# Performance work log

Measured on AMD Instinct MI355X. Metric: run time of the kernel, lower is better.

## Reference

```python
import jax, jax.numpy as jnp
import numpy as np

B, L, D, S = 64, 512, 768, 8
HOP, LAMB = 3, 0.5


def _layernorm(x, g, b, eps=1e-5):
    m = x.mean(-1, keepdims=True)
    v = x.var(-1, keepdims=True)
    return (x - m) / jnp.sqrt(v + eps) * g + b


def _hop_refine(cur, sentence, ln_g, ln_b):
    # cur, sentence: [B,S,D]. HOP-1 refinement steps, then return last row.
    for _ in range(HOP - 1):
        coef = jnp.einsum('bd,bsd->bs', cur[:, -1, :], sentence)  # [B,S]
        a = coef[..., None] * sentence                             # [B,S,D]
        cur = LAMB * _layernorm(jax.nn.sigmoid(a), ln_g, ln_b) + sentence
    return cur[:, -1, :]  # [B,D]


def _conv1d(x, w, b):
    # x: [B,D,S], w: [Dout,Din,3], padding=1 (same)
    y = jax.lax.conv_general_dilated(
        x, w, window_strides=(1,), padding=((1, 1),),
        dimension_numbers=('NCH', 'OIH', 'NCH'))
    return y + b[None, :, None]


def setup_inputs() -> dict:
    key = jax.random.key(0)
    ks = jax.random.split(key, 16)
    p = lambda k, shp: (jax.random.normal(k, shp, dtype=jnp.float32) * 0.02)
    # segment boundaries: strictly increasing, start at 1, <= L, gaps ~63 with jitter < 32
    base = 1 + np.arange(S + 1) * ((L - 1) // S)          # [9]
    jitter = np.array(jax.random.randint(ks[15], (B, S + 1), 0, 32))
    jitter[:, 0] = 0
    jitter[:, -1] = 0
    seg_bounds = jnp.asarray(base[None, :] + jitter, dtype=jnp.int64 if jax.config.jax_enable_x64 else jnp.int32)
    return {
        'bert_output': jax.random.normal(ks[0], (B, L, D), dtype=jnp.float32),
        'target': jax.random.normal(ks[1], (B, D), dtype=jnp.float32),
        'gc1_w': p(ks[2], (D, D)), 'gc1_b': p(ks[3], (D,)),
        'gc2_w': p(ks[4], (D, D)), 'gc2_b': p(ks[5], (D,)),
        'conv1_w': p(ks[6], (D, D, 3)), 'conv1_b': p(ks[7], (D,)),
        'conv2_w': p(ks[8], (D, D, 3)), 'conv2_b': p(ks[9], (D,)),
        'ln_g': jnp.ones((D,), jnp.float32), 'ln_b': jnp.zeros((D,), jnp.float32),
        'fc2_w': p(ks[10], (3 * D, 3)), 'fc2_b': p(ks[11], (3,)),
        'seg_bounds': seg_bounds,
    }


def reference(bert_output, target, gc1_w, gc1_b, gc2_w, gc2_b,
              conv1_w, conv1_b, conv2_w, conv2_b, ln_g, ln_b,
              fc2_w, fc2_b, seg_bounds):
    dt = bert_output.dtype
    start = seg_bounds[:, :-1]   # [B,S]
    end = seg_bounds[:, 1:]      # [B,S]
    pos = jnp.arange(L)
    seg_mask = ((pos[None, None, :] >= start[:, :, None]) &
                (pos[None, None, :] < end[:, :, None])).astype(dt)  # [B,S,L]
    cnt = (end - start).astype(dt)                                   # [B,S]
    # batched segment-mean pooling
    sentence = jnp.einsum('bsl,bld->bsd', seg_mask, bert_output) / cnt[..., None]

    # GCN branch: adj = I + superdiagonal, row-degree normalization
    adj = jnp.eye(S, dtype=dt) + jnp.eye(S, k=1, dtype=dt)
    denom = adj.sum(axis=1)  # [S]

    def gcn(x, w, b):
        h = jnp.einsum('bsd,de->bse', x, w)
        return jnp.einsum('st,btd->bsd', adj, h) / denom[None, :, None] + b

    g1 = jnp.tanh(gcn(sentence, gc1_w, gc1_b))
    g2 = jnp.tanh(gcn(g1, gc2_w, gc2_b))
    a3 = _hop_refine(g2, sentence, ln_g, ln_b)

    # Conv branch: two conv1d (k=3, pad=1) over the segment axis
    x = jnp.swapaxes(sentence, 1, 2)  # [B,D,S]
    c = jnp.tanh(_conv1d(x, conv1_w, conv1_b))
    c = jnp.tanh(_conv1d(c, conv2_w, conv2_b))
    conv_out = jnp.swapaxes(c, 1, 2)  # [B,S,D]
    a4 = _hop_refine(conv_out, sentence, ln_g, ln_b)

    # Self-mask branch
    coef0 = jnp.einsum('bd,bsd->bs', sentence[:, -1, :], sentence)
    tmask = jax.nn.sigmoid(coef0[..., None] * sentence)
    a5 = _hop_refine(tmask, sentence, ln_g, ln_b)

    fnout = jnp.stack([a3, a4, a5], axis=1)                 # [B,3,D]
    # NOTE: original uses target[0] (first sample's pooler output) for all samples
    w = jax.nn.softmax(jnp.einsum('bkd,d->bk', fnout, target[0]), axis=1)
    fn = (fnout * w[..., None]).reshape(fnout.shape[0], 3 * D)
    return fn @ fc2_w + fc2_b  # [B,3]
```

## Files before the change

### kernel.cpp

```cpp
#include <hip/hip_runtime.h>


typedef unsigned short u16;
typedef short short8 __attribute__((ext_vector_type(8)));
typedef float f32x4 __attribute__((ext_vector_type(4)));

#define PSLAB 147456

__device__ __forceinline__ float bf2f(u16 h) {
    unsigned int u = ((unsigned int)h) << 16;
    float f;
    __builtin_memcpy(&f, &u, 4);
    return f;
}
__device__ __forceinline__ u16 f2bf(float f) {
    unsigned int u;
    __builtin_memcpy(&u, &f, 4);
    u = (u + 0x7fffu + ((u >> 16) & 1u)) >> 16;
    return (u16)u;
}
__device__ __forceinline__ float sigm(float x) { return 1.0f / (1.0f + __expf(-x)); }

__device__ __forceinline__ float ldv(const void* p, long i, bool bf) {
    return bf ? bf2f(((const u16*)p)[i]) : ((const float*)p)[i];
}

__device__ __forceinline__ bool detect_bf16(const u16* bert) {
    int hits = 0;
#pragma unroll
    for (int i = 0; i < 256; i += 2) {
        const int e = (bert[i] >> 7) & 0xFF;
        hits += (e >= 115 && e <= 130) ? 1 : 0;
    }
    return hits > 64;
}

template <int NSUM, int ACT, int WMODE>
__device__ __forceinline__ void gemm_core(
    const float* __restrict__ x, int xstride, int pslab,
    const void* __restrict__ bias, const void* __restrict__ W, bool bf,
    float* __restrict__ out, int ostride,
    int n0, int k0, int kiters, u16* As, u16* Bs)
{
    const int t = threadIdx.x;
    const int r = t >> 2;
    const int cseg = (t & 3) * 32;
    const int wave = t >> 6, lane = t & 63;
    const int lm = lane & 15, lq = lane >> 4;
    f32x4 acc[4] = {};

    for (int kk = 0; kk < kiters * 128; kk += 128) {
        const int kg = k0 + kk;
        {
            const float* xp = x + (size_t)r * xstride + (kg + cseg);
            u16* dst = As + r * 136 + cseg;
#pragma unroll
            for (int i = 0; i < 8; ++i) {
                float4 v = ((const float4*)xp)[i];
#pragma unroll
                for (int sfx = 1; sfx < NSUM; ++sfx) {
                    float4 vv = ((const float4*)(xp + (size_t)sfx * pslab))[i];
                    v.x += vv.x; v.y += vv.y; v.z += vv.z; v.w += vv.w;
                }
                if (ACT) {
                    int kb = kg + cseg + i * 4;
                    if (kb >= 768) kb -= 768;
                    v.x = tanhf(v.x + ldv(bias, kb, bf));
                    v.y = tanhf(v.y + ldv(bias, kb + 1, bf));
                    v.z = tanhf(v.z + ldv(bias, kb + 2, bf));
                    v.w = tanhf(v.w + ldv(bias, kb + 3, bf));
                }
                ((ushort4*)dst)[i] = make_ushort4(f2bf(v.x), f2bf(v.y), f2bf(v.z), f2bf(v.w));
            }
        }
        if (WMODE == 0) {
            const int p = t >> 2;
            const int nseg = (t & 3) * 16;
            u16 q0[16], q1[16];
            if (bf) {
                const u16* w0 = (const u16*)W + (size_t)(kg + 2 * p) * 768 + n0 + nseg;
                ((uint4*)q0)[0] = ((const uint4*)w0)[0];
                ((uint4*)q0)[1] = ((const uint4*)w0)[1];
                ((uint4*)q1)[0] = ((const uint4*)(w0 + 768))[0];
                ((uint4*)q1)[1] = ((const uint4*)(w0 + 768))[1];
            } else {
                const float* w0 = (const float*)W + (size_t)(kg + 2 * p) * 768 + n0 + nseg;
#pragma unroll
                for (int e = 0; e < 4; ++e) {
                    float4 v0 = ((const float4*)w0)[e];
                    float4 v1 = ((const float4*)(w0 + 768))[e];
                    q0[4 * e] = f2bf(v0.x); q0[4 * e + 1] = f2bf(v0.y);
                    q0[4 * e + 2] = f2bf(v0.z); q0[4 * e + 3] = f2bf(v0.w);
                    q1[4 * e] = f2bf(v1.x); q1[4 * e + 1] = f2bf(v1.y);
                    q1[4 * e + 2] = f2bf(v1.z); q1[4 * e + 3] = f2bf(v1.w);
                }
            }
#pragma unroll
            for (int e = 0; e < 16; ++e)
                *(ushort2*)(Bs + (nseg + e) * 136 + 2 * p) = make_ushort2(q0[e], q1[e]);
        } else {
            const int kb = kg / 768;
            const int i0c = kg - kb * 768;
            u16 tmp[32];
            if (bf) {
                const u16* wp = (const u16*)W + (size_t)(n0 + r) * 2304 + (size_t)(i0c + cseg) * 3 + kb;
#pragma unroll
                for (int j = 0; j < 32; ++j) tmp[j] = wp[j * 3];
            } else {
                const float* wp = (const float*)W + (size_t)(n0 + r) * 2304 + (size_t)(i0c + cseg) * 3 + kb;
#pragma unroll
                for (int j = 0; j < 32; ++j) tmp[j] = f2bf(wp[j * 3]);
            }
            u16* dst = Bs + r * 136 + cseg;
#pragma unroll
            for (int qq = 0; qq < 8; ++qq)
                ((ushort4*)dst)[qq] = ((ushort4*)tmp)[qq];
        }
        __syncthreads();
        const u16* ap = As + (wave * 16 + lm) * 136 + lq * 8;
        const u16* bp = Bs + lm * 136 + lq * 8;
#pragma unroll
        for (int ks = 0; ks < 4; ++ks) {
            short8 af = *(const short8*)(ap + ks * 32);
#pragma unroll
            for (int nf = 0; nf < 4; ++nf) {
                short8 bfr = *(const short8*)(bp + nf * 16 * 136 + ks * 32);
                acc[nf] = __builtin_amdgcn_mfma_f32_16x16x32_bf16(af, bfr, acc[nf], 0, 0, 0);
            }
        }
        __syncthreads();
    }
#pragma unroll
    for (int nf = 0; nf < 4; ++nf) {
#pragma unroll
        for (int rg = 0; rg < 4; ++rg) {
            const int row = wave * 16 + lq * 4 + rg;
            const int col = n0 + nf * 16 + lm;
            out[(size_t)row * ostride + col] = acc[nf][rg];
        }
    }
}

__device__ __forceinline__ float block_sum(float v, float* red) {
#pragma unroll
    for (int m = 1; m < 64; m <<= 1) v += __shfl_xor(v, m, 64);
    const int wave = threadIdx.x >> 6, lane = threadIdx.x & 63;
    if (lane == 0) red[wave] = v;
    __syncthreads();
    const float r = red[0] + red[1] + red[2] + red[3];
    __syncthreads();
    return r;
}

__global__ __launch_bounds__(256) void kA_pool(
    const void* __restrict__ bertv, const int* __restrict__ sb,
    float* __restrict__ sentP)
{
    const int u = blockIdx.x, t = threadIdx.x;
    const bool bf = detect_bf16((const u16*)bertv);
    const bool is64 = (sb[1] == 0);
    const int q = u & 3, v = u >> 2;
    const int b = v / 3, si = v - 3 * (v / 3), s = 5 + si;
    const int i0 = b * 9 + s, i1 = i0 + 1;
    int st = is64 ? sb[2 * i0] : sb[i0];
    int en = is64 ? sb[2 * i1] : sb[i1];
    st = st < 0 ? 0 : (st > 511 ? 511 : st);
    en = en <= st ? st + 1 : (en > 512 ? 512 : en);
    const int n = en - st;
    const int r0 = st + (n * q) / 4;
    const int r1 = st + (n * (q + 1)) / 4;
    float a0 = 0.f, a1 = 0.f, a2 = 0.f;
    if (bf) {
        const u16* base = (const u16*)bertv + (size_t)b * 512 * 768;
        int l = r0;
        for (; l + 1 < r1; l += 2) {
            const u16* p0 = base + (size_t)l * 768;
            const u16* p1 = p0 + 768;
            a0 += bf2f(p0[t]) + bf2f(p1[t]);
            a1 += bf2f(p0[t + 256]) + bf2f(p1[t + 256]);
            a2 += bf2f(p0[t + 512]) + bf2f(p1[t + 512]);
        }
        if (l < r1) {
            const u16* p0 = base + (size_t)l * 768;
            a0 += bf2f(p0[t]);
            a1 += bf2f(p0[t + 256]);
            a2 += bf2f(p0[t + 512]);
        }
    } else {
        const float* base = (const float*)bertv + (size_t)b * 512 * 768;
        int l = r0;
        for (; l + 1 < r1; l += 2) {
            const float* p0 = base + (size_t)l * 768;
            const float* p1 = p0 + 768;
            a0 += p0[t] + p1[t];
            a1 += p0[t + 256] + p1[t + 256];
            a2 += p0[t + 512] + p1[t + 512];
        }
        if (l < r1) {
            const float* p0 = base + (size_t)l * 768;
            a0 += p0[t];
            a1 += p0[t + 256];
            a2 += p0[t + 512];
        }
    }
    const float inv = 1.0f / (float)n;
    float* o = sentP + (size_t)q * PSLAB + b * 2304 + si * 768;
    o[t] = a0 * inv;
    o[t + 256] = a1 * inv;
    o[t + 512] = a2 * inv;
}

__global__ __launch_bounds__(256) void kB_gemm_a(
    const float* __restrict__ sentP, const void* __restrict__ bertv,
    const void* __restrict__ gc1w, const void* __restrict__ c1w,
    float* __restrict__ g1p, float* __restrict__ c1p)
{
    __shared__ u16 As[64 * 136];
    __shared__ u16 Bs[64 * 136];
    const bool bf = detect_bf16((const u16*)bertv);
    const int u = blockIdx.x;
    if (u < 36) {
        const int nt = u / 3, jc = u % 3;
        gemm_core<4, 0, 0>(sentP + 1536, 2304, PSLAB, nullptr, gc1w, bf,
                           g1p + jc * 49152, 768, nt * 64, jc * 256, 2, As, Bs);
    } else if (u < 108) {
        const int v = u - 36, nt = v / 6, jc = v % 6;
        gemm_core<4, 0, 1>(sentP, 2304, PSLAB, nullptr, c1w, bf,
                           c1p + jc * 98304, 1536, nt * 64, jc * 384, 3, As, Bs);
    } else {
        const int v = u - 108, nt = v / 6, jc = v % 6;
        gemm_core<4, 0, 1>(sentP + 768, 2304, PSLAB, nullptr, c1w, bf,
                           c1p + jc * 98304 + 768, 1536, nt * 64, jc * 256, 2, As, Bs);
    }
}

__global__ __launch_bounds__(256) void kC_gemm_b(
    const float* __restrict__ g1p, const float* __restrict__ c1p,
    const void* __restrict__ bertv,
    const void* __restrict__ gc2w, const void* __restrict__ c2w,
    const void* __restrict__ gc1b, const void* __restrict__ c1b,
    float* __restrict__ g2p, float* __restrict__ c2p)
{
    __shared__ u16 As[64 * 136];
    __shared__ u16 Bs[64 * 136];
    const bool bf = detect_bf16((const u16*)bertv);
    const int u = blockIdx.x;
    if (u < 36) {
        const int nt = u / 3, jc = u % 3;
        gemm_core<3, 1, 0>(g1p, 768, 49152, gc1b, gc2w, bf,
                           g2p + jc * 49152, 768, nt * 64, jc * 256, 2, As, Bs);
    } else {
        const int v = u - 36, nt = v / 4, jc = v % 4;
        gemm_core<6, 1, 1>(c1p, 1536, 98304, c1b, c2w, bf,
                           c2p + jc * 49152, 768, nt * 64, jc * 384, 3, As, Bs);
    }
}

__global__ __launch_bounds__(256) void kD_final(
    const float* __restrict__ sentP, const float* __restrict__ g2p,
    const float* __restrict__ c2p, const void* __restrict__ bertv,
    const void* __restrict__ gc2b, const void* __restrict__ c2b,
    const void* __restrict__ lng, const void* __restrict__ lnb,
    const void* __restrict__ target, const void* __restrict__ fc2w,
    const void* __restrict__ fc2b, void* __restrict__ outp)
{
    __shared__ float red[4];
    const bool bf = detect_bf16((const u16*)bertv);
    const int t = threadIdx.x, b = blockIdx.x;
    float s_[3], g_[3], bb_[3];
    const float* srow = sentP + b * 2304 + 1536;
#pragma unroll
    for (int i = 0; i < 3; ++i) {
        const int d = t + 256 * i;
        s_[i] = srow[d] + srow[d + PSLAB] + srow[d + 2 * PSLAB] + srow[d + 3 * PSLAB];
        g_[i] = ldv(lng, d, bf);
        bb_[i] = ldv(lnb, d, bf);
    }

    auto refine2 = [&](float* yv) {
#pragma unroll
        for (int it = 0; it < 2; ++it) {
            const float c = block_sum(yv[0] * s_[0] + yv[1] * s_[1] + yv[2] * s_[2], red);
            float tt[3], sm = 0.0f, sq = 0.0f;
#pragma unroll
            for (int i = 0; i < 3; ++i) {
                tt[i] = sigm(c * s_[i]);
                sm += tt[i];
                sq += tt[i] * tt[i];
            }
            const float m = block_sum(sm, red) * (1.0f / 768.0f);
            const float q = block_sum(sq, red) * (1.0f / 768.0f);
            const float inv = rsqrtf(fmaxf(q - m * m, 0.0f) + 1e-5f);
#pragma unroll
            for (int i = 0; i < 3; ++i)
                yv[i] = 0.5f * ((tt[i] - m) * inv * g_[i] + bb_[i]) + s_[i];
        }
    };

    float a3[3], a4[3], a5[3], y[3];
#pragma unroll
    for (int i = 0; i < 3; ++i) {
        const int d = t + 256 * i;
        const float gs = g2p[b * 768 + d] + g2p[49152 + b * 768 + d] + g2p[98304 + b * 768 + d];
        y[i] = tanhf(gs + ldv(gc2b, d, bf));
    }
    refine2(y);
    a3[0] = y[0]; a3[1] = y[1]; a3[2] = y[2];
#pragma unroll
    for (int i = 0; i < 3; ++i) {
        const int d = t + 256 * i;
        const float cs = c2p[b * 768 + d] + c2p[49152 + b * 768 + d]
                       + c2p[98304 + b * 768 + d] + c2p[147456 + b * 768 + d];
        y[i] = tanhf(cs + ldv(c2b, d, bf));
    }
    refine2(y);
    a4[0] = y[0]; a4[1] = y[1]; a4[2] = y[2];
    const float ss = block_sum(s_[0] * s_[0] + s_[1] * s_[1] + s_[2] * s_[2], red);
#pragma unroll
    for (int i = 0; i < 3; ++i) y[i] = sigm(ss * s_[i]);
    refine2(y);
    a5[0] = y[0]; a5[1] = y[1]; a5[2] = y[2];

    float tg[3];
#pragma unroll
    for (int i = 0; i < 3; ++i) tg[i] = ldv(target, t + 256 * i, bf);
    const float u0 = block_sum(a3[0] * tg[0] + a3[1] * tg[1] + a3[2] * tg[2], red);
    const float u1 = block_sum(a4[0] * tg[0] + a4[1] * tg[1] + a4[2] * tg[2], red);
    const float u2 = block_sum(a5[0] * tg[0] + a5[1] * tg[1] + a5[2] * tg[2], red);
    const float mx = fmaxf(u0, fmaxf(u1, u2));
    const float e0 = __expf(u0 - mx), e1 = __expf(u1 - mx), e2 = __expf(u2 - mx);
    const float es = e0 + e1 + e2;
    const float w0 = e0 / es, w1 = e1 / es, w2 = e2 / es;

    float p0 = 0.0f, p1 = 0.0f, p2 = 0.0f;
#pragma unroll
    for (int i = 0; i < 3; ++i) {
        const int d = t + 256 * i;
        const float va = w0 * a3[i], vb = w1 * a4[i], vc = w2 * a5[i];
        p0 += va * ldv(fc2w, d * 3 + 0, bf) + vb * ldv(fc2w, (768 + d) * 3 + 0, bf) + vc * ldv(fc2w, (1536 + d) * 3 + 0, bf);
        p1 += va * ldv(fc2w, d * 3 + 1, bf) + vb * ldv(fc2w, (768 + d) * 3 + 1, bf) + vc * ldv(fc2w, (1536 + d) * 3 + 1, bf);
        p2 += va * ldv(fc2w, d * 3 + 2, bf) + vb * ldv(fc2w, (768 + d) * 3 + 2, bf) + vc * ldv(fc2w, (1536 + d) * 3 + 2, bf);
    }
    p0 = block_sum(p0, red);
    p1 = block_sum(p1, red);
    p2 = block_sum(p2, red);
    if (t == 0) {
        const float o0 = p0 + ldv(fc2b, 0, bf);
        const float o1 = p1 + ldv(fc2b, 1, bf);
        const float o2 = p2 + ldv(fc2b, 2, bf);
        if (bf) {
            ((u16*)outp)[b * 3 + 0] = f2bf(o0);
            ((u16*)outp)[b * 3 + 1] = f2bf(o1);
            ((u16*)outp)[b * 3 + 2] = f2bf(o2);
        } else {
            ((float*)outp)[b * 3 + 0] = o0;
            ((float*)outp)[b * 3 + 1] = o1;
            ((float*)outp)[b * 3 + 2] = o2;
        }
    }
}

extern "C" void kernel_launch(void* const* d_in, const int* in_sizes, int n_in,
                              void* d_out, int out_size, void* d_ws, size_t ws_size,
                              hipStream_t stream) {
    const void* bert   = d_in[0];
    const void* target = d_in[1];
    const void* gc1w   = d_in[2];
    const void* gc1b   = d_in[3];
    const void* gc2w   = d_in[4];
    const void* gc2b   = d_in[5];
    const void* c1w    = d_in[6];
    const void* c1b    = d_in[7];
    const void* c2w    = d_in[8];
    const void* c2b    = d_in[9];
    const void* lng    = d_in[10];
    const void* lnb    = d_in[11];
    const void* fc2w   = d_in[12];
    const void* fc2b   = d_in[13];
    const int*  sb     = (const int*)d_in[14];

    float* sentP = (float*)d_ws;
    float* g1p   = sentP + 4 * PSLAB;
    float* c1p   = g1p + 147456;
    float* g2p   = c1p + 589824;
    float* c2p   = g2p + 147456;

    kA_pool<<<768, 256, 0, stream>>>(bert, sb, sentP);
    kB_gemm_a<<<180, 256, 0, stream>>>(sentP, bert, gc1w, c1w, g1p, c1p);
    kC_gemm_b<<<84, 256, 0, stream>>>(g1p, c1p, bert, gc2w, c2w, gc1b, c1b, g2p, c2p);
    kD_final<<<64, 256, 0, stream>>>(sentP, g2p, c2p, bert, gc2b, c2b, lng, lnb,
                                     target, fc2w, fc2b, d_out);
}
```

Measured before the change: 266.5 us.

## Use atomic split-K accumulation in GEMMs and wave-per-sample final kernel

GEMM partial sums are now accumulated with atomicAdd into zeroed fp32 buffers instead of being written to separate per-split slabs that later stages had to sum. The accumulators are zeroed inside the pooling kernel. Split-K is made uniform at two 128-wide chunks, which raises block counts. The final kernel processes one sample per wavefront using shuffle-only reductions instead of block-wide LDS reductions with syncthreads. Atomics make the summation order nondeterministic and add contention on the output buffers.

```diff
diff --git a/kernel.cpp b/kernel.cpp
--- a/kernel.cpp
+++ b/kernel.cpp
@@ -35,12 +35,12 @@
     return hits > 64;
 }
 
-template <int NSUM, int ACT, int WMODE>
+template <int XMODE, int WMODE>
 __device__ __forceinline__ void gemm_core(
     const float* __restrict__ x, int xstride, int pslab,
     const void* __restrict__ bias, const void* __restrict__ W, bool bf,
     float* __restrict__ out, int ostride,
-    int n0, int k0, int kiters, u16* As, u16* Bs)
+    int n0, int k0, u16* As, u16* Bs)
 {
     const int t = threadIdx.x;
     const int r = t >> 2;
@@ -49,7 +49,7 @@
     const int lm = lane & 15, lq = lane >> 4;
     f32x4 acc[4] = {};
 
-    for (int kk = 0; kk < kiters * 128; kk += 128) {
+    for (int kk = 0; kk < 256; kk += 128) {
         const int kg = k0 + kk;
         {
             const float* xp = x + (size_t)r * xstride + (kg + cseg);
@@ -57,12 +57,16 @@
 #pragma unroll
             for (int i = 0; i < 8; ++i) {
                 float4 v = ((const float4*)xp)[i];
-#pragma unroll
-                for (int sfx = 1; sfx < NSUM; ++sfx) {
-                    float4 vv = ((const float4*)(xp + (size_t)sfx * pslab))[i];
-                    v.x += vv.x; v.y += vv.y; v.z += vv.z; v.w += vv.w;
+                if (XMODE == 2) {
+                    float4 v1 = ((const float4*)(xp + pslab))[i];
+                    float4 v2 = ((const float4*)(xp + 2 * pslab))[i];
+                    float4 v3 = ((const float4*)(xp + 3 * pslab))[i];
+                    v.x += v1.x + v2.x + v3.x;
+                    v.y += v1.y + v2.y + v3.y;
+                    v.z += v1.z + v2.z + v3.z;
+                    v.w += v1.w + v2.w + v3.w;
                 }
-                if (ACT) {
+                if (XMODE == 1) {
                     int kb = kg + cseg + i * 4;
                     if (kb >= 768) kb -= 768;
                     v.x = tanhf(v.x + ldv(bias, kb, bf));
@@ -136,27 +140,18 @@
         for (int rg = 0; rg < 4; ++rg) {
             const int row = wave * 16 + lq * 4 + rg;
             const int col = n0 + nf * 16 + lm;
-            out[(size_t)row * ostride + col] = acc[nf][rg];
-        }
-    }
-}
-
-__device__ __forceinline__ float block_sum(float v, float* red) {
-#pragma unroll
-    for (int m = 1; m < 64; m <<= 1) v += __shfl_xor(v, m, 64);
-    const int wave = threadIdx.x >> 6, lane = threadIdx.x & 63;
-    if (lane == 0) red[wave] = v;
-    __syncthreads();
-    const float r = red[0] + red[1] + red[2] + red[3];
-    __syncthreads();
-    return r;
+            atomicAdd(out + (size_t)row * ostride + col, acc[nf][rg]);
+        }
+    }
 }
 
 __global__ __launch_bounds__(256) void kA_pool(
     const void* __restrict__ bertv, const int* __restrict__ sb,
-    float* __restrict__ sentP)
+    float* __restrict__ sentP, float* __restrict__ accs)
 {
     const int u = blockIdx.x, t = threadIdx.x;
+    if (t < 80)
+        ((float4*)accs)[u * 80 + t] = make_float4(0.f, 0.f, 0.f, 0.f);
     const bool bf = detect_bf16((const u16*)bertv);
     const bool is64 = (sb[1] == 0);
     const int q = u & 3, v = u >> 2;
@@ -213,65 +208,70 @@
 __global__ __launch_bounds__(256) void kB_gemm_a(
     const float* __restrict__ sentP, const void* __restrict__ bertv,
     const void* __restrict__ gc1w, const void* __restrict__ c1w,
-    float* __restrict__ g1p, float* __restrict__ c1p)
+    float* __restrict__ g1acc, float* __restrict__ c1acc)
 {
     __shared__ u16 As[64 * 136];
     __shared__ u16 Bs[64 * 136];
     const bool bf = detect_bf16((const u16*)bertv);
     const int u = blockIdx.x;
     if (u < 36) {
-        const int nt = u / 3, jc = u % 3;
-        gemm_core<4, 0, 0>(sentP + 1536, 2304, PSLAB, nullptr, gc1w, bf,
-                           g1p + jc * 49152, 768, nt * 64, jc * 256, 2, As, Bs);
-    } else if (u < 108) {
-        const int v = u - 36, nt = v / 6, jc = v % 6;
-        gemm_core<4, 0, 1>(sentP, 2304, PSLAB, nullptr, c1w, bf,
-                           c1p + jc * 98304, 1536, nt * 64, jc * 384, 3, As, Bs);
+        gemm_core<2, 0>(sentP + 1536, 2304, PSLAB, nullptr, gc1w, bf, g1acc, 768,
+                        (u / 3) * 64, (u % 3) * 256, As, Bs);
+    } else if (u < 144) {
+        const int v = u - 36;
+        gemm_core<2, 1>(sentP, 2304, PSLAB, nullptr, c1w, bf, c1acc, 1536,
+                        (v / 9) * 64, (v % 9) * 256, As, Bs);
     } else {
-        const int v = u - 108, nt = v / 6, jc = v % 6;
-        gemm_core<4, 0, 1>(sentP + 768, 2304, PSLAB, nullptr, c1w, bf,
-                           c1p + jc * 98304 + 768, 1536, nt * 64, jc * 256, 2, As, Bs);
+        const int v = u - 144;
+        gemm_core<2, 1>(sentP + 768, 2304, PSLAB, nullptr, c1w, bf, c1acc + 768, 1536,
+                        (v / 6) * 64, (v % 6) * 256, As, Bs);
     }
 }
 
 __global__ __launch_bounds__(256) void kC_gemm_b(
-    const float* __restrict__ g1p, const float* __restrict__ c1p,
+    const float* __restrict__ g1acc, const float* __restrict__ c1acc,
     const void* __restrict__ bertv,
     const void* __restrict__ gc2w, const void* __restrict__ c2w,
     const void* __restrict__ gc1b, const void* __restrict__ c1b,
-    float* __restrict__ g2p, float* __restrict__ c2p)
+    float* __restrict__ g2acc, float* __restrict__ c2acc)
 {
     __shared__ u16 As[64 * 136];
     __shared__ u16 Bs[64 * 136];
     const bool bf = detect_bf16((const u16*)bertv);
     const int u = blockIdx.x;
     if (u < 36) {
-        const int nt = u / 3, jc = u % 3;
-        gemm_core<3, 1, 0>(g1p, 768, 49152, gc1b, gc2w, bf,
-                           g2p + jc * 49152, 768, nt * 64, jc * 256, 2, As, Bs);
+        gemm_core<1, 0>(g1acc, 768, 0, gc1b, gc2w, bf, g2acc, 768,
+                        (u / 3) * 64, (u % 3) * 256, As, Bs);
     } else {
-        const int v = u - 36, nt = v / 4, jc = v % 4;
-        gemm_core<6, 1, 1>(c1p, 1536, 98304, c1b, c2w, bf,
-                           c2p + jc * 49152, 768, nt * 64, jc * 384, 3, As, Bs);
-    }
+        const int v = u - 36;
+        gemm_core<1, 1>(c1acc, 1536, 0, c1b, c2w, bf, c2acc, 768,
+                        (v / 6) * 64, (v % 6) * 256, As, Bs);
+    }
+}
+
+__device__ __forceinline__ float wsum(float v) {
+#pragma unroll
+    for (int m = 1; m < 64; m <<= 1) v += __shfl_xor(v, m, 64);
+    return v;
 }
 
 __global__ __launch_bounds__(256) void kD_final(
-    const float* __restrict__ sentP, const float* __restrict__ g2p,
-    const float* __restrict__ c2p, const void* __restrict__ bertv,
+    const float* __restrict__ sentP, const float* __restrict__ g2acc,
+    const float* __restrict__ c2acc, const void* __restrict__ bertv,
     const void* __restrict__ gc2b, const void* __restrict__ c2b,
     const void* __restrict__ lng, const void* __restrict__ lnb,
     const void* __restrict__ target, const void* __restrict__ fc2w,
     const void* __restrict__ fc2b, void* __restrict__ outp)
 {
-    __shared__ float red[4];
     const bool bf = detect_bf16((const u16*)bertv);
-    const int t = threadIdx.x, b = blockIdx.x;
-    float s_[3], g_[3], bb_[3];
+    const int t = threadIdx.x, wave = t >> 6, lane = t & 63;
+    const int b = blockIdx.x * 4 + wave;
+
+    float s_[12], g_[12], bb_[12];
     const float* srow = sentP + b * 2304 + 1536;
 #pragma unroll
-    for (int i = 0; i < 3; ++i) {
-        const int d = t + 256 * i;
+    for (int i = 0; i < 12; ++i) {
+        const int d = lane + 64 * i;
         s_[i] = srow[d] + srow[d + PSLAB] + srow[d + 2 * PSLAB] + srow[d + 3 * PSLAB];
         g_[i] = ldv(lng, d, bf);
         bb_[i] = ldv(lnb, d, bf);
@@ -280,53 +280,62 @@
     auto refine2 = [&](float* yv) {
 #pragma unroll
         for (int it = 0; it < 2; ++it) {
-            const float c = block_sum(yv[0] * s_[0] + yv[1] * s_[1] + yv[2] * s_[2], red);
-            float tt[3], sm = 0.0f, sq = 0.0f;
-#pragma unroll
-            for (int i = 0; i < 3; ++i) {
+            float cacc = 0.f;
+#pragma unroll
+            for (int i = 0; i < 12; ++i) cacc += yv[i] * s_[i];
+            const float c = wsum(cacc);
+            float tt[12], sm = 0.0f, sq = 0.0f;
+#pragma unroll
+            for (int i = 0; i < 12; ++i) {
                 tt[i] = sigm(c * s_[i]);
                 sm += tt[i];
                 sq += tt[i] * tt[i];
             }
-            const float m = block_sum(sm, red) * (1.0f / 768.0f);
-            const float q = block_sum(sq, red) * (1.0f / 768.0f);
+            const float m = wsum(sm) * (1.0f / 768.0f);
+            const float q = wsum(sq) * (1.0f / 768.0f);
             const float inv = rsqrtf(fmaxf(q - m * m, 0.0f) + 1e-5f);
 #pragma unroll
-            for (int i = 0; i < 3; ++i)
+            for (int i = 0; i < 12; ++i)
                 yv[i] = 0.5f * ((tt[i] - m) * inv * g_[i] + bb_[i]) + s_[i];
         }
     };
 
-    float a3[3], a4[3], a5[3], y[3];
-#pragma unroll
-    for (int i = 0; i < 3; ++i) {
-        const int d = t + 256 * i;
-        const float gs = g2p[b * 768 + d] + g2p[49152 + b * 768 + d] + g2p[98304 + b * 768 + d];
-        y[i] = tanhf(gs + ldv(gc2b, d, bf));
+    float a3[12], a4[12], a5[12], y[12];
+#pragma unroll
+    for (int i = 0; i < 12; ++i) {
+        const int d = lane + 64 * i;
+        y[i] = tanhf(g2acc[b * 768 + d] + ldv(gc2b, d, bf));
     }
     refine2(y);
-    a3[0] = y[0]; a3[1] = y[1]; a3[2] = y[2];
-#pragma unroll
-    for (int i = 0; i < 3; ++i) {
-        const int d = t + 256 * i;
-        const float cs = c2p[b * 768 + d] + c2p[49152 + b * 768 + d]
-                       + c2p[98304 + b * 768 + d] + c2p[147456 + b * 768 + d];
-        y[i] = tanhf(cs + ldv(c2b, d, bf));
+#pragma unroll
+    for (int i = 0; i < 12; ++i) a3[i] = y[i];
+#pragma unroll
+    for (int i = 0; i < 12; ++i) {
+        const int d = lane + 64 * i;
+        y[i] = tanhf(c2acc[b * 768 + d] + ldv(c2b, d, bf));
     }
     refine2(y);
-    a4[0] = y[0]; a4[1] = y[1]; a4[2] = y[2];
-    const float ss = block_sum(s_[0] * s_[0] + s_[1] * s_[1] + s_[2] * s_[2], red);
-#pragma unroll
-    for (int i = 0; i < 3; ++i) y[i] = sigm(ss * s_[i]);
+#pragma unroll
+    for (int i = 0; i < 12; ++i) a4[i] = y[i];
+    float ssacc = 0.f;
+#pragma unroll
+    for (int i = 0; i < 12; ++i) ssacc += s_[i] * s_[i];
+    const float ss = wsum(ssacc);
+#pragma unroll
+    for (int i = 0; i < 12; ++i) y[i] = sigm(ss * s_[i]);
     refine2(y);
-    a5[0] = y[0]; a5[1] = y[1]; a5[2] = y[2];
-
-    float tg[3];
-#pragma unroll
-    for (int i = 0; i < 3; ++i) tg[i] = ldv(target, t + 256 * i, bf);
-    const float u0 = block_sum(a3[0] * tg[0] + a3[1] * tg[1] + a3[2] * tg[2], red);
-    const float u1 = block_sum(a4[0] * tg[0] + a4[1] * tg[1] + a4[2] * tg[2], red);
-    const float u2 = block_sum(a5[0] * tg[0] + a5[1] * tg[1] + a5[2] * tg[2], red);
+#pragma unroll
+    for (int i = 0; i < 12; ++i) a5[i] = y[i];
+
+    float d0 = 0.f, d1 = 0.f, d2 = 0.f;
+#pragma unroll
+    for (int i = 0; i < 12; ++i) {
+        const float tg = ldv(target, lane + 64 * i, bf);
+        d0 += a3[i] * tg;
+        d1 += a4[i] * tg;
+        d2 += a5[i] * tg;
+    }
+    const float u0 = wsum(d0), u1 = wsum(d1), u2 = wsum(d2);
     const float mx = fmaxf(u0, fmaxf(u1, u2));
     const float e0 = __expf(u0 - mx), e1 = __expf(u1 - mx), e2 = __expf(u2 - mx);
     const float es = e0 + e1 + e2;
@@ -334,17 +343,17 @@
 
     float p0 = 0.0f, p1 = 0.0f, p2 = 0.0f;
 #pragma unroll
-    for (int i = 0; i < 3; ++i) {
-        const int d = t + 256 * i;
+    for (int i = 0; i < 12; ++i) {
+        const int d = lane + 64 * i;
         const float va = w0 * a3[i], vb = w1 * a4[i], vc = w2 * a5[i];
         p0 += va * ldv(fc2w, d * 3 + 0, bf) + vb * ldv(fc2w, (768 + d) * 3 + 0, bf) + vc * ldv(fc2w, (1536 + d) * 3 + 0, bf);
         p1 += va * ldv(fc2w, d * 3 + 1, bf) + vb * ldv(fc2w, (768 + d) * 3 + 1, bf) + vc * ldv(fc2w, (1536 + d) * 3 + 1, bf);
         p2 += va * ldv(fc2w, d * 3 + 2, bf) + vb * ldv(fc2w, (768 + d) * 3 + 2, bf) + vc * ldv(fc2w, (1536 + d) * 3 + 2, bf);
     }
-    p0 = block_sum(p0, red);
-    p1 = block_sum(p1, red);
-    p2 = block_sum(p2, red);
-    if (t == 0) {
+    p0 = wsum(p0);
+    p1 = wsum(p1);
+    p2 = wsum(p2);
+    if (lane == 0) {
         const float o0 = p0 + ldv(fc2b, 0, bf);
         const float o1 = p1 + ldv(fc2b, 1, bf);
         const float o2 = p2 + ldv(fc2b, 2, bf);
@@ -380,14 +389,15 @@
     const int*  sb     = (const int*)d_in[14];
 
     float* sentP = (float*)d_ws;
-    float* g1p   = sentP + 4 * PSLAB;
-    float* c1p   = g1p + 147456;
-    float* g2p   = c1p + 589824;
-    float* c2p   = g2p + 147456;
-
-    kA_pool<<<768, 256, 0, stream>>>(bert, sb, sentP);
-    kB_gemm_a<<<180, 256, 0, stream>>>(sentP, bert, gc1w, c1w, g1p, c1p);
-    kC_gemm_b<<<84, 256, 0, stream>>>(g1p, c1p, bert, gc2w, c2w, gc1b, c1b, g2p, c2p);
-    kD_final<<<64, 256, 0, stream>>>(sentP, g2p, c2p, bert, gc2b, c2b, lng, lnb,
+    float* accs  = sentP + 4 * PSLAB;
+    float* g1acc = accs;
+    float* c1acc = accs + 49152;
+    float* g2acc = c1acc + 98304;
+    float* c2acc = g2acc + 49152;
+
+    kA_pool<<<768, 256, 0, stream>>>(bert, sb, sentP, accs);
+    kB_gemm_a<<<216, 256, 0, stream>>>(sentP, bert, gc1w, c1w, g1acc, c1acc);
+    kC_gemm_b<<<108, 256, 0, stream>>>(g1acc, c1acc, bert, gc2w, c2w, gc1b, c1b, g2acc, c2acc);
+    kD_final<<<16, 256, 0, stream>>>(sentP, g2acc, c2acc, bert, gc2b, c2b, lng, lnb,
                                      target, fc2w, fc2b, d_out);
 }
```

After: 245.0 us. 1.09x faster.
